# Performance work log

Measured on AMD Instinct MI355X. Metric: run time of the kernel, lower is better.

## Reference

```python
import jax, jax.numpy as jnp
import numpy as np
import math

L, B, T, D, H, F = 4, 4, 2048, 1024, 1024, 256
R_MIN, R_MAX = 0.9, 0.99
MAX_PHASE = math.pi / 50  # hardcoded in LRU.__init__


def setup_inputs() -> dict:
    key = jax.random.key(0)
    ks = iter(jax.random.split(key, 32))
    inputs = jax.random.normal(next(ks), (B, T, F), dtype=jnp.float32)
    # input projection (torch Linear layout: W [out,in])
    lim = 1.0 / math.sqrt(F)
    W_in = jax.random.uniform(next(ks), (D, F), minval=-lim, maxval=lim, dtype=jnp.float32)
    b_in = jax.random.uniform(next(ks), (D,), minval=-lim, maxval=lim, dtype=jnp.float32)
    # per-layer LRU params (stacked over layer dim)
    u1 = jax.random.uniform(next(ks), (L, H), dtype=jnp.float32) * (1 - 1e-5) + 1e-5
    mag_sq = u1 * (R_MAX ** 2 - R_MIN ** 2) + R_MIN ** 2
    nu_log = jnp.log(-0.5 * jnp.log(mag_sq + 1e-5))
    u2 = jax.random.uniform(next(ks), (L, H), dtype=jnp.float32) * (1 - 1e-5) + 1e-5
    theta_log = jnp.log(MAX_PHASE * u2)
    B_re = jax.random.normal(next(ks), (L, H, D), dtype=jnp.float32) / math.sqrt(2 * D)
    B_im = jax.random.normal(next(ks), (L, H, D), dtype=jnp.float32) / math.sqrt(2 * D)
    C_re = jax.random.normal(next(ks), (L, D, H), dtype=jnp.float32) / math.sqrt(H)
    C_im = jax.random.normal(next(ks), (L, D, H), dtype=jnp.float32) / math.sqrt(H)
    D_diag = jax.random.normal(next(ks), (L, D), dtype=jnp.float32)
    # LayerNorm affine
    ln_scale = jnp.ones((L, D), dtype=jnp.float32)
    ln_bias = jnp.zeros((L, D), dtype=jnp.float32)
    # GLU output linears (torch layout [out,in])
    limd = 1.0 / math.sqrt(D)
    w1 = jax.random.uniform(next(ks), (L, D, D), minval=-limd, maxval=limd, dtype=jnp.float32)
    b1 = jax.random.uniform(next(ks), (L, D), minval=-limd, maxval=limd, dtype=jnp.float32)
    w2 = jax.random.uniform(next(ks), (L, D, D), minval=-limd, maxval=limd, dtype=jnp.float32)
    b2 = jax.random.uniform(next(ks), (L, D), minval=-limd, maxval=limd, dtype=jnp.float32)
    return {"inputs": inputs, "W_in": W_in, "b_in": b_in, "nu_log": nu_log,
            "theta_log": theta_log, "B_re": B_re, "B_im": B_im, "C_re": C_re,
            "C_im": C_im, "D_diag": D_diag, "ln_scale": ln_scale, "ln_bias": ln_bias,
            "w1": w1, "b1": b1, "w2": w2, "b2": b2}


def _layernorm(x, scale, bias, eps=1e-5):
    mu = jnp.mean(x, axis=-1, keepdims=True)
    var = jnp.mean((x - mu) ** 2, axis=-1, keepdims=True)
    return (x - mu) * jax.lax.rsqrt(var + eps) * scale + bias


def _lru(x, nu_log, theta_log, B_re, B_im, C_re, C_im, D_diag):
    # x: [B,T,D] real -> [B,T,D] real
    nu = jnp.exp(nu_log)
    theta = jnp.exp(theta_log)
    lam = jnp.exp(-nu + 1j * theta)                        # [H] complex
    # gamma recomputed from nu_log each forward (matches torch code)
    gamma = jnp.exp(0.5 * jnp.log(1 - jnp.exp(-2 * nu) + 1e-5))
    B_norm = (B_re + 1j * B_im) * gamma[:, None]           # [H,D]
    Bu = jnp.einsum('hd,btd->bth', B_norm, x.astype(jnp.complex64))  # [B,T,H]

    def step(h, bu):
        h = lam * h + bu
        return h, h

    h0 = jnp.zeros((x.shape[0], lam.shape[0]), dtype=jnp.complex64)
    _, hs = jax.lax.scan(step, h0, jnp.swapaxes(Bu, 0, 1))  # [T,B,H]
    hs = jnp.swapaxes(hs, 0, 1)                             # [B,T,H]
    C = C_re + 1j * C_im                                    # [D,H]
    y = jnp.einsum('bth,dh->btd', hs, C).real + x * D_diag
    return y.astype(jnp.float32)


def reference(inputs, W_in, b_in, nu_log, theta_log, B_re, B_im, C_re, C_im,
              D_diag, ln_scale, ln_bias, w1, b1, w2, b2):
    x = inputs @ W_in.T + b_in                              # [B,T,D]
    n_layers = nu_log.shape[0]
    for l in range(n_layers):
        xn = _layernorm(x, ln_scale[l], ln_bias[l])
        y = _lru(xn, nu_log[l], theta_log[l], B_re[l], B_im[l],
                 C_re[l], C_im[l], D_diag[l])
        y = jax.nn.gelu(y, approximate=False)
        y = (y @ w1[l].T + b1[l]) * jax.nn.sigmoid(y @ w2[l].T + b2[l])
        x = x + y
    return x
```

## Files before the change

### kernel.cpp

```cpp
#include <hip/hip_runtime.h>
#include <hip/hip_bf16.h>
#include <math.h>

typedef unsigned short u16;
typedef short s16x8 __attribute__((ext_vector_type(8)));
typedef float f32x4 __attribute__((ext_vector_type(4)));
typedef unsigned short u16x4 __attribute__((ext_vector_type(4)));

#define NLAYER 4
#define BB 4
#define TT 2048
#define DD 1024
#define HH 1024
#define FF 256
#define MM 8192
#define CL 64
#define NC 32
#define PLANE 4096
#define STPLANE 131072

__device__ __forceinline__ u16 f2bf(float f) {
  __hip_bfloat16 h = __float2bfloat16(f);
  return __builtin_bit_cast(u16, h);
}
__device__ __forceinline__ float bf2f(u16 u) {
  __hip_bfloat16 h = __builtin_bit_cast(__hip_bfloat16, u);
  return __bfloat162float(h);
}

__global__ __launch_bounds__(256) void params_kernel(
    const float* __restrict__ nu_log, const float* __restrict__ theta_log,
    float* __restrict__ P) {
  int i = blockIdx.x * 256 + threadIdx.x;
  if (i >= PLANE) return;
  float nu = expf(nu_log[i]);
  float th = expf(theta_log[i]);
  float r = expf(-nu);
  P[i]           = r * cosf(th);
  P[PLANE + i]   = r * sinf(th);
  P[2*PLANE + i] = sqrtf(1.f - expf(-2.f * nu) + 1e-5f);
  float rC = expf(-(float)CL * nu);
  float thC = (float)CL * th;
  P[3*PLANE + i] = rC * cosf(thC);
  P[4*PLANE + i] = rC * sinf(thC);
}

__global__ __launch_bounds__(256) void f2bf_kernel(
    const float* __restrict__ src, u16* __restrict__ dst, int n) {
  int i = blockIdx.x * 256 + threadIdx.x;
  if (i < n) dst[i] = f2bf(src[i]);
}

__global__ __launch_bounds__(256) void conv_layer_kernel(
    const float* __restrict__ Bre, const float* __restrict__ Bim,
    const float* __restrict__ Cre, const float* __restrict__ Cim,
    const float* __restrict__ w1, const float* __restrict__ w2,
    const float* __restrict__ gamma,
    u16* __restrict__ wBn, u16* __restrict__ wC,
    u16* __restrict__ w1b, u16* __restrict__ w2b) {
  int idx = blockIdx.x * 256 + threadIdx.x;
  if (idx < 2097152) {
    int n = idx >> 10, d = idx & 1023;
    float v = (n < 1024) ? Bre[n * 1024 + d] * gamma[n]
                         : Bim[(n - 1024) * 1024 + d] * gamma[n - 1024];
    wBn[idx] = f2bf(v);
  } else if (idx < 4194304) {
    int i = idx - 2097152;
    int d = i >> 11, k = i & 2047;
    float v = (k < 1024) ? Cre[d * 1024 + k] : -Cim[d * 1024 + (k - 1024)];
    wC[i] = f2bf(v);
  } else if (idx < 5242880) {
    int i = idx - 4194304;
    w1b[i] = f2bf(w1[i]);
  } else if (idx < 6291456) {
    int i = idx - 5242880;
    w2b[i] = f2bf(w2[i]);
  }
}

__global__ __launch_bounds__(256) void ln_kernel(
    const float* __restrict__ x, const float* __restrict__ sc,
    const float* __restrict__ bi, u16* __restrict__ xn) {
  const int row = blockIdx.x;
  const int tid = threadIdx.x;
  const float4 v = ((const float4*)(x + (size_t)row * 1024))[tid];
  float s = v.x + v.y + v.z + v.w;
  float ss = v.x * v.x + v.y * v.y + v.z * v.z + v.w * v.w;
  __shared__ float r1[256], r2[256];
  r1[tid] = s; r2[tid] = ss;
  __syncthreads();
  for (int stp = 128; stp > 0; stp >>= 1) {
    if (tid < stp) { r1[tid] += r1[tid + stp]; r2[tid] += r2[tid + stp]; }
    __syncthreads();
  }
  const float mu = r1[0] * 0.0009765625f;
  const float var = r2[0] * 0.0009765625f - mu * mu;
  const float inv = rsqrtf(var + 1e-5f);
  const int c = tid * 4;
  u16x4 o;
  o.x = f2bf((v.x - mu) * inv * sc[c]     + bi[c]);
  o.y = f2bf((v.y - mu) * inv * sc[c + 1] + bi[c + 1]);
  o.z = f2bf((v.z - mu) * inv * sc[c + 2] + bi[c + 2]);
  o.w = f2bf((v.w - mu) * inv * sc[c + 3] + bi[c + 3]);
  *(u16x4*)&xn[(size_t)row * 1024 + c] = o;
}

__global__ __launch_bounds__(256) void scanA_kernel(
    u16* __restrict__ Bu, const float* __restrict__ P, float* __restrict__ st,
    int l) {
  const int tid = blockIdx.x * 256 + threadIdx.x;
  const int h2 = tid & 511;
  const int c = (tid >> 9) & 31;
  const int b = tid >> 14;
  const int h = h2 * 2;
  const float lr0 = P[l * 1024 + h],     li0 = P[PLANE + l * 1024 + h];
  const float lr1 = P[l * 1024 + h + 1], li1 = P[PLANE + l * 1024 + h + 1];
  const size_t base = ((size_t)(b * TT + c * CL)) * 2048 + h;
  float h0r = 0.f, h0i = 0.f, h1r = 0.f, h1i = 0.f;
  for (int j = 0; j < CL; j++) {
    size_t o = base + (size_t)j * 2048;
    uint re2 = *(const uint*)(Bu + o);
    uint im2 = *(const uint*)(Bu + o + 1024);
    float b0r = bf2f((u16)(re2 & 0xffffu)), b1r = bf2f((u16)(re2 >> 16));
    float b0i = bf2f((u16)(im2 & 0xffffu)), b1i = bf2f((u16)(im2 >> 16));
    float t0r = lr0 * h0r - li0 * h0i + b0r;
    float t0i = lr0 * h0i + li0 * h0r + b0i;
    float t1r = lr1 * h1r - li1 * h1i + b1r;
    float t1i = lr1 * h1i + li1 * h1r + b1i;
    h0r = t0r; h0i = t0i; h1r = t1r; h1i = t1i;
    *(uint*)(Bu + o)        = (uint)f2bf(h0r) | ((uint)f2bf(h1r) << 16);
    *(uint*)(Bu + o + 1024) = (uint)f2bf(h0i) | ((uint)f2bf(h1i) << 16);
  }
  size_t si = ((size_t)(b * NC + c)) * 1024 + h;
  st[si] = h0r; st[si + 1] = h1r;
  st[STPLANE + si] = h0i; st[STPLANE + si + 1] = h1i;
}

__global__ __launch_bounds__(256) void scanB_kernel(
    float* __restrict__ st, const float* __restrict__ P, int l) {
  const int tid = blockIdx.x * 256 + threadIdx.x;
  const int h = tid & 1023;
  const int b = tid >> 10;
  const float cr = P[3*PLANE + l * 1024 + h], ci = P[4*PLANE + l * 1024 + h];
  float pr = 0.f, pi = 0.f;
  for (int c = 0; c < NC; c++) {
    size_t i = ((size_t)(b * NC + c)) * 1024 + h;
    float sr = st[i], sim = st[STPLANE + i];
    st[i] = pr; st[STPLANE + i] = pi;
    float nr = cr * pr - ci * pi + sr;
    float ni = cr * pi + ci * pr + sim;
    pr = nr; pi = ni;
  }
}

__global__ __launch_bounds__(256) void scanC_kernel(
    u16* __restrict__ Bu, const float* __restrict__ P,
    const float* __restrict__ st, int l) {
  const int tid = blockIdx.x * 256 + threadIdx.x;
  const int h2 = tid & 511;
  const int c = (tid >> 9) & 31;
  const int b = tid >> 14;
  if (c == 0) return;
  const int h = h2 * 2;
  const float lr0 = P[l * 1024 + h],     li0 = P[PLANE + l * 1024 + h];
  const float lr1 = P[l * 1024 + h + 1], li1 = P[PLANE + l * 1024 + h + 1];
  size_t si = ((size_t)(b * NC + c)) * 1024 + h;
  float q0r = st[si], q1r = st[si + 1];
  float q0i = st[STPLANE + si], q1i = st[STPLANE + si + 1];
  const size_t base = ((size_t)(b * TT + c * CL)) * 2048 + h;
  for (int j = 0; j < CL; j++) {
    float t0r = lr0 * q0r - li0 * q0i;
    float t0i = lr0 * q0i + li0 * q0r;
    float t1r = lr1 * q1r - li1 * q1i;
    float t1i = lr1 * q1i + li1 * q1r;
    q0r = t0r; q0i = t0i; q1r = t1r; q1i = t1i;
    size_t o = base + (size_t)j * 2048;
    uint re2 = *(const uint*)(Bu + o);
    uint im2 = *(const uint*)(Bu + o + 1024);
    float v0r = bf2f((u16)(re2 & 0xffffu)) + q0r;
    float v1r = bf2f((u16)(re2 >> 16))     + q1r;
    float v0i = bf2f((u16)(im2 & 0xffffu)) + q0i;
    float v1i = bf2f((u16)(im2 >> 16))     + q1i;
    *(uint*)(Bu + o)        = (uint)f2bf(v0r) | ((uint)f2bf(v1r) << 16);
    *(uint*)(Bu + o + 1024) = (uint)f2bf(v0i) | ((uint)f2bf(v1i) << 16);
  }
}

__device__ __forceinline__ void stage_rows(const u16* __restrict__ gbase,
                                           int row_stride, u16* lds_base,
                                           int rows_per_wave, int wave,
                                           int lane) {
  const int r8 = lane >> 3;
  const int slot = lane & 7;
  const int gc = (slot ^ r8) * 8;
  #pragma unroll
  for (int i = 0; i < rows_per_wave / 8; i++) {
    const int rbase = wave * rows_per_wave + i * 8;
    const u16* g = gbase + (size_t)(rbase + r8) * row_stride + gc;
    u16* l = lds_base + rbase * 64;
    __builtin_amdgcn_global_load_lds(
        (const __attribute__((address_space(1))) void*)g,
        (__attribute__((address_space(3))) void*)l, 16, 0, 0);
  }
}

template <int MODE>
__global__ __launch_bounds__(256, 4) void gemm_kernel(
    const u16* __restrict__ A, const u16* __restrict__ W,
    const u16* __restrict__ W2, int K, int N, void* __restrict__ outp,
    const float* __restrict__ bias, const float* __restrict__ bias2,
    const float* __restrict__ ddiag, const u16* __restrict__ xnp) {
  __shared__ u16 As[128 * 64];
  __shared__ u16 Bs[64 * 64];
  __shared__ u16 Bs2[(MODE == 3) ? 64 * 64 : 64];

  const int tid = threadIdx.x;
  const int m0 = blockIdx.x * 128;
  const int n0 = blockIdx.y * 64;
  const int wave = tid >> 6;
  const int lane = tid & 63;
  const int wm = wave & 1;
  const int wn = wave >> 1;
  const int lr = lane & 15;
  const int quad = lane >> 4;
  const int sw = lr & 7;

  f32x4 acc[4][2];
  f32x4 acc2[4][2];
  #pragma unroll
  for (int i = 0; i < 4; i++)
    #pragma unroll
    for (int j = 0; j < 2; j++)
      #pragma unroll
      for (int r = 0; r < 4; r++) {
        acc[i][j][r] = 0.f;
        if constexpr (MODE == 3) acc2[i][j][r] = 0.f;
      }

  for (int kb = 0; kb < K; kb += 64) {
    stage_rows(A + (size_t)m0 * K + kb, K, As, 32, wave, lane);
    stage_rows(W + (size_t)n0 * K + kb, K, Bs, 16, wave, lane);
    if constexpr (MODE == 3)
      stage_rows(W2 + (size_t)n0 * K + kb, K, Bs2, 16, wave, lane);
    __syncthreads();
    #pragma unroll
    for (int ks = 0; ks < 2; ks++) {
      const int cslot = ((ks * 4 + quad) ^ sw) * 8;
      s16x8 af[4], bfr[2], bfr2[2];
      #pragma unroll
      for (int t = 0; t < 4; t++)
        af[t] = *(const s16x8*)&As[(wm * 64 + t * 16 + lr) * 64 + cslot];
      #pragma unroll
      for (int t = 0; t < 2; t++) {
        bfr[t] = *(const s16x8*)&Bs[(wn * 32 + t * 16 + lr) * 64 + cslot];
        if constexpr (MODE == 3)
          bfr2[t] = *(const s16x8*)&Bs2[(wn * 32 + t * 16 + lr) * 64 + cslot];
      }
      #pragma unroll
      for (int mt = 0; mt < 4; mt++)
        #pragma unroll
        for (int nt = 0; nt < 2; nt++) {
          acc[mt][nt] = __builtin_amdgcn_mfma_f32_16x16x32_bf16(
              af[mt], bfr[nt], acc[mt][nt], 0, 0, 0);
          if constexpr (MODE == 3)
            acc2[mt][nt] = __builtin_amdgcn_mfma_f32_16x16x32_bf16(
                af[mt], bfr2[nt], acc2[mt][nt], 0, 0, 0);
        }
    }
    __syncthreads();
  }

  const int mbase = m0 + wm * 64 + quad * 4;
  const int nbase = n0 + wn * 32 + lr;
  #pragma unroll
  for (int mt = 0; mt < 4; mt++)
    #pragma unroll
    for (int nt = 0; nt < 2; nt++) {
      const int n = nbase + nt * 16;
      #pragma unroll
      for (int r = 0; r < 4; r++) {
        const int m = mbase + mt * 16 + r;
        const float v = acc[mt][nt][r];
        if constexpr (MODE == 0) {
          ((u16*)outp)[(size_t)m * N + n] = f2bf(v);
        } else if constexpr (MODE == 1) {
          ((float*)outp)[(size_t)m * N + n] = v + bias[n];
        } else if constexpr (MODE == 2) {
          float t = v + bf2f(xnp[(size_t)m * 1024 + n]) * ddiag[n];
          float g = t * 0.5f * (1.f + erff(t * 0.70710678118f));
          ((u16*)outp)[(size_t)m * N + n] = f2bf(g);
        } else {
          float a = v + bias[n];
          float g2 = acc2[mt][nt][r] + bias2[n];
          float sig = 1.f / (1.f + expf(-g2));
          float* xp = (float*)outp;
          xp[(size_t)m * N + n] += a * sig;
        }
      }
    }
}

extern "C" void kernel_launch(void* const* d_in, const int* in_sizes, int n_in,
                              void* d_out, int out_size, void* d_ws,
                              size_t ws_size, hipStream_t stream) {
  const float* inputs    = (const float*)d_in[0];
  const float* W_in      = (const float*)d_in[1];
  const float* b_in      = (const float*)d_in[2];
  const float* nu_log    = (const float*)d_in[3];
  const float* theta_log = (const float*)d_in[4];
  const float* B_re      = (const float*)d_in[5];
  const float* B_im      = (const float*)d_in[6];
  const float* C_re      = (const float*)d_in[7];
  const float* C_im      = (const float*)d_in[8];
  const float* D_diag    = (const float*)d_in[9];
  const float* ln_s      = (const float*)d_in[10];
  const float* ln_b      = (const float*)d_in[11];
  const float* w1        = (const float*)d_in[12];
  const float* b1        = (const float*)d_in[13];
  const float* w2        = (const float*)d_in[14];
  const float* b2        = (const float*)d_in[15];
  float* x = (float*)d_out;

  char* p = (char*)d_ws;
  auto alloc = [&](size_t bytes) -> char* {
    char* r = p;
    p += (bytes + 255) & ~(size_t)255;
    return r;
  };
  float* P       = (float*)alloc(5 * PLANE * 4);
  u16* inputs_bf = (u16*)alloc((size_t)MM * FF * 2);
  u16* Win_bf    = (u16*)alloc((size_t)DD * FF * 2);
  u16* xn        = (u16*)alloc((size_t)MM * DD * 2);
  u16* Bu        = (u16*)alloc((size_t)MM * 2048 * 2);
  u16* yg        = (u16*)alloc((size_t)MM * DD * 2);
  float* st      = (float*)alloc(2 * (size_t)STPLANE * 4);
  u16* wBn       = (u16*)alloc((size_t)2048 * 1024 * 2);
  u16* wC        = (u16*)alloc((size_t)1024 * 2048 * 2);
  u16* w1b       = (u16*)alloc((size_t)1024 * 1024 * 2);
  u16* w2b       = (u16*)alloc((size_t)1024 * 1024 * 2);

  params_kernel<<<16, 256, 0, stream>>>(nu_log, theta_log, P);
  f2bf_kernel<<<(MM * FF + 255) / 256, 256, 0, stream>>>(inputs, inputs_bf, MM * FF);
  f2bf_kernel<<<(DD * FF + 255) / 256, 256, 0, stream>>>(W_in, Win_bf, DD * FF);

  gemm_kernel<1><<<dim3(64, 16), 256, 0, stream>>>(
      inputs_bf, Win_bf, nullptr, FF, DD, x, b_in, nullptr, nullptr, nullptr);

  for (int l = 0; l < NLAYER; l++) {
    ln_kernel<<<MM, 256, 0, stream>>>(x, ln_s + l * 1024, ln_b + l * 1024, xn);
    conv_layer_kernel<<<24576, 256, 0, stream>>>(
        B_re + (size_t)l * 1048576, B_im + (size_t)l * 1048576,
        C_re + (size_t)l * 1048576, C_im + (size_t)l * 1048576,
        w1 + (size_t)l * 1048576, w2 + (size_t)l * 1048576,
        P + 2 * PLANE + l * 1024, wBn, wC, w1b, w2b);
    gemm_kernel<0><<<dim3(64, 32), 256, 0, stream>>>(
        xn, wBn, nullptr, DD, 2048, Bu, nullptr, nullptr, nullptr, nullptr);
    scanA_kernel<<<256, 256, 0, stream>>>(Bu, P, st, l);
    scanB_kernel<<<16, 256, 0, stream>>>(st, P, l);
    scanC_kernel<<<256, 256, 0, stream>>>(Bu, P, st, l);
    gemm_kernel<2><<<dim3(64, 16), 256, 0, stream>>>(
        Bu, wC, nullptr, 2048, DD, yg, nullptr, nullptr, D_diag + l * 1024, xn);
    gemm_kernel<3><<<dim3(64, 16), 256, 0, stream>>>(
        yg, w1b, w2b, DD, DD, x, b1 + l * 1024, b2 + l * 1024, nullptr, nullptr);
  }
}
```

Before: 954.5 us.

## Double-buffer GEMM LDS tiles, remap blocks to 1D grid, split GLU GEMM

The GEMM kernel now keeps two LDS buffers per operand and prefetches the next K tile while computing the current one, which drops one barrier per iteration. Blocks are launched on a flat 1D grid and remapped so that consecutive groups of blocks fall on different XCD-strided tile ranges, aiming at better L2 locality. The fused dual-weight GLU GEMM is split into two passes: a sigmoid-gate GEMM that writes bf16 into the Bu buffer, then a value GEMM that multiplies by the stored gate and accumulates into x. The split lowers register pressure but adds an extra activation round-trip, and launch bounds drop to 3 blocks per SM to fit the doubled LDS.

```diff
diff --git a/kernel.cpp b/kernel.cpp
--- a/kernel.cpp
+++ b/kernel.cpp
@@ -205,18 +205,23 @@
 }
 
 template <int MODE>
-__global__ __launch_bounds__(256, 4) void gemm_kernel(
+__global__ __launch_bounds__(256, 3) void gemm_kernel(
     const u16* __restrict__ A, const u16* __restrict__ W,
-    const u16* __restrict__ W2, int K, int N, void* __restrict__ outp,
-    const float* __restrict__ bias, const float* __restrict__ bias2,
+    int K, int N, void* __restrict__ outp,
+    const float* __restrict__ bias,
     const float* __restrict__ ddiag, const u16* __restrict__ xnp) {
-  __shared__ u16 As[128 * 64];
-  __shared__ u16 Bs[64 * 64];
-  __shared__ u16 Bs2[(MODE == 3) ? 64 * 64 : 64];
+  __shared__ u16 As[2][128 * 64];
+  __shared__ u16 Bs[2][64 * 64];
 
   const int tid = threadIdx.x;
-  const int m0 = blockIdx.x * 128;
-  const int n0 = blockIdx.y * 64;
+  const int total = gridDim.x;
+  const int per = total >> 3;
+  const int flat = blockIdx.x;
+  const int g2 = (flat & 7) * per + (flat >> 3);
+  const int NT = N >> 6;
+  const int m0 = (g2 / NT) * 128;
+  const int n0 = (g2 % NT) * 64;
+
   const int wave = tid >> 6;
   const int lane = tid & 63;
   const int wm = wave & 1;
@@ -226,48 +231,44 @@
   const int sw = lr & 7;
 
   f32x4 acc[4][2];
-  f32x4 acc2[4][2];
   #pragma unroll
   for (int i = 0; i < 4; i++)
     #pragma unroll
     for (int j = 0; j < 2; j++)
       #pragma unroll
-      for (int r = 0; r < 4; r++) {
-        acc[i][j][r] = 0.f;
-        if constexpr (MODE == 3) acc2[i][j][r] = 0.f;
-      }
-
-  for (int kb = 0; kb < K; kb += 64) {
-    stage_rows(A + (size_t)m0 * K + kb, K, As, 32, wave, lane);
-    stage_rows(W + (size_t)n0 * K + kb, K, Bs, 16, wave, lane);
-    if constexpr (MODE == 3)
-      stage_rows(W2 + (size_t)n0 * K + kb, K, Bs2, 16, wave, lane);
+      for (int r = 0; r < 4; r++) acc[i][j][r] = 0.f;
+
+  const u16* Abase = A + (size_t)m0 * K;
+  const u16* Wbase = W + (size_t)n0 * K;
+  const int KI = K >> 6;
+
+  stage_rows(Abase, K, As[0], 32, wave, lane);
+  stage_rows(Wbase, K, Bs[0], 16, wave, lane);
+
+  for (int ki = 0; ki < KI; ki++) {
+    const int cur = ki & 1;
     __syncthreads();
+    if (ki + 1 < KI) {
+      stage_rows(Abase + ((ki + 1) << 6), K, As[cur ^ 1], 32, wave, lane);
+      stage_rows(Wbase + ((ki + 1) << 6), K, Bs[cur ^ 1], 16, wave, lane);
+    }
     #pragma unroll
     for (int ks = 0; ks < 2; ks++) {
       const int cslot = ((ks * 4 + quad) ^ sw) * 8;
-      s16x8 af[4], bfr[2], bfr2[2];
+      s16x8 af[4], bfr[2];
       #pragma unroll
       for (int t = 0; t < 4; t++)
-        af[t] = *(const s16x8*)&As[(wm * 64 + t * 16 + lr) * 64 + cslot];
-      #pragma unroll
-      for (int t = 0; t < 2; t++) {
-        bfr[t] = *(const s16x8*)&Bs[(wn * 32 + t * 16 + lr) * 64 + cslot];
-        if constexpr (MODE == 3)
-          bfr2[t] = *(const s16x8*)&Bs2[(wn * 32 + t * 16 + lr) * 64 + cslot];
-      }
+        af[t] = *(const s16x8*)&As[cur][(wm * 64 + t * 16 + lr) * 64 + cslot];
+      #pragma unroll
+      for (int t = 0; t < 2; t++)
+        bfr[t] = *(const s16x8*)&Bs[cur][(wn * 32 + t * 16 + lr) * 64 + cslot];
       #pragma unroll
       for (int mt = 0; mt < 4; mt++)
         #pragma unroll
-        for (int nt = 0; nt < 2; nt++) {
+        for (int nt = 0; nt < 2; nt++)
           acc[mt][nt] = __builtin_amdgcn_mfma_f32_16x16x32_bf16(
               af[mt], bfr[nt], acc[mt][nt], 0, 0, 0);
-          if constexpr (MODE == 3)
-            acc2[mt][nt] = __builtin_amdgcn_mfma_f32_16x16x32_bf16(
-                af[mt], bfr2[nt], acc2[mt][nt], 0, 0, 0);
-        }
     }
-    __syncthreads();
   }
 
   const int mbase = m0 + wm * 64 + quad * 4;
@@ -289,12 +290,12 @@
           float t = v + bf2f(xnp[(size_t)m * 1024 + n]) * ddiag[n];
           float g = t * 0.5f * (1.f + erff(t * 0.70710678118f));
           ((u16*)outp)[(size_t)m * N + n] = f2bf(g);
+        } else if constexpr (MODE == 4) {
+          float sig = 1.f / (1.f + expf(-(v + bias[n])));
+          ((u16*)outp)[(size_t)m * N + n] = f2bf(sig);
         } else {
           float a = v + bias[n];
-          float g2 = acc2[mt][nt][r] + bias2[n];
-          float sig = 1.f / (1.f + expf(-g2));
-          float* xp = (float*)outp;
-          xp[(size_t)m * N + n] += a * sig;
+          ((float*)outp)[(size_t)m * N + n] += a * bf2f(xnp[(size_t)m * N + n]);
         }
       }
     }
@@ -338,13 +339,14 @@
   u16* wC        = (u16*)alloc((size_t)1024 * 2048 * 2);
   u16* w1b       = (u16*)alloc((size_t)1024 * 1024 * 2);
   u16* w2b       = (u16*)alloc((size_t)1024 * 1024 * 2);
+  u16* sg        = Bu;
 
   params_kernel<<<16, 256, 0, stream>>>(nu_log, theta_log, P);
   f2bf_kernel<<<(MM * FF + 255) / 256, 256, 0, stream>>>(inputs, inputs_bf, MM * FF);
   f2bf_kernel<<<(DD * FF + 255) / 256, 256, 0, stream>>>(W_in, Win_bf, DD * FF);
 
-  gemm_kernel<1><<<dim3(64, 16), 256, 0, stream>>>(
-      inputs_bf, Win_bf, nullptr, FF, DD, x, b_in, nullptr, nullptr, nullptr);
+  gemm_kernel<1><<<1024, 256, 0, stream>>>(
+      inputs_bf, Win_bf, FF, DD, x, b_in, nullptr, nullptr);
 
   for (int l = 0; l < NLAYER; l++) {
     ln_kernel<<<MM, 256, 0, stream>>>(x, ln_s + l * 1024, ln_b + l * 1024, xn);
@@ -353,14 +355,16 @@
         C_re + (size_t)l * 1048576, C_im + (size_t)l * 1048576,
         w1 + (size_t)l * 1048576, w2 + (size_t)l * 1048576,
         P + 2 * PLANE + l * 1024, wBn, wC, w1b, w2b);
-    gemm_kernel<0><<<dim3(64, 32), 256, 0, stream>>>(
-        xn, wBn, nullptr, DD, 2048, Bu, nullptr, nullptr, nullptr, nullptr);
+    gemm_kernel<0><<<2048, 256, 0, stream>>>(
+        xn, wBn, DD, 2048, Bu, nullptr, nullptr, nullptr);
     scanA_kernel<<<256, 256, 0, stream>>>(Bu, P, st, l);
     scanB_kernel<<<16, 256, 0, stream>>>(st, P, l);
     scanC_kernel<<<256, 256, 0, stream>>>(Bu, P, st, l);
-    gemm_kernel<2><<<dim3(64, 16), 256, 0, stream>>>(
-        Bu, wC, nullptr, 2048, DD, yg, nullptr, nullptr, D_diag + l * 1024, xn);
-    gemm_kernel<3><<<dim3(64, 16), 256, 0, stream>>>(
-        yg, w1b, w2b, DD, DD, x, b1 + l * 1024, b2 + l * 1024, nullptr, nullptr);
-  }
-}
+    gemm_kernel<2><<<1024, 256, 0, stream>>>(
+        Bu, wC, 2048, DD, yg, nullptr, D_diag + l * 1024, xn);
+    gemm_kernel<4><<<1024, 256, 0, stream>>>(
+        yg, w2b, DD, DD, sg, b2 + l * 1024, nullptr, nullptr);
+    gemm_kernel<5><<<1024, 256, 0, stream>>>(
+        yg, w1b, DD, DD, x, b1 + l * 1024, nullptr, sg);
+  }
+}
```

Measured after the change: 1.231 ms. +28.9%, slower.

## Use 2-wave GEMM blocks with 64x64 per-wave tiles and XCD-aware block remap

Applied to the files above, without the earlier changes.

Each GEMM block now runs 2 waves instead of 4, and each wave computes a 64x64 tile (4x4 MFMA subtiles) rather than 64x32, which raises the MFMA work per LDS fragment load. The 2D grid is flattened and remapped so that consecutive block groups land on the same XCD (flat&7 stride), improving L2 locality across the 8 chiplets. The larger per-wave tile raises register pressure, especially in MODE 3 where both acc arrays double. Halving the threads per block also doubles the staging work each thread does.

```diff
diff --git a/kernel.cpp b/kernel.cpp
--- a/kernel.cpp
+++ b/kernel.cpp
@@ -205,7 +205,7 @@
 }
 
 template <int MODE>
-__global__ __launch_bounds__(256, 4) void gemm_kernel(
+__global__ __launch_bounds__(128, (MODE == 3) ? 2 : 3) void gemm_kernel(
     const u16* __restrict__ A, const u16* __restrict__ W,
     const u16* __restrict__ W2, int K, int N, void* __restrict__ outp,
     const float* __restrict__ bias, const float* __restrict__ bias2,
@@ -215,51 +215,55 @@
   __shared__ u16 Bs2[(MODE == 3) ? 64 * 64 : 64];
 
   const int tid = threadIdx.x;
-  const int m0 = blockIdx.x * 128;
-  const int n0 = blockIdx.y * 64;
+  const int per = gridDim.x >> 3;
+  const int flat = blockIdx.x;
+  const int g2 = (flat & 7) * per + (flat >> 3);
+  const int NT = N >> 6;
+  const int m0 = (g2 / NT) * 128;
+  const int n0 = (g2 % NT) * 64;
+
   const int wave = tid >> 6;
   const int lane = tid & 63;
-  const int wm = wave & 1;
-  const int wn = wave >> 1;
   const int lr = lane & 15;
   const int quad = lane >> 4;
   const int sw = lr & 7;
 
-  f32x4 acc[4][2];
-  f32x4 acc2[4][2];
+  f32x4 acc[4][4];
+  f32x4 acc2[4][4];
   #pragma unroll
   for (int i = 0; i < 4; i++)
     #pragma unroll
-    for (int j = 0; j < 2; j++)
+    for (int j = 0; j < 4; j++)
       #pragma unroll
       for (int r = 0; r < 4; r++) {
         acc[i][j][r] = 0.f;
         if constexpr (MODE == 3) acc2[i][j][r] = 0.f;
       }
 
+  const u16* Abase = A + (size_t)m0 * K;
+  const u16* Wbase = W + (size_t)n0 * K;
+
   for (int kb = 0; kb < K; kb += 64) {
-    stage_rows(A + (size_t)m0 * K + kb, K, As, 32, wave, lane);
-    stage_rows(W + (size_t)n0 * K + kb, K, Bs, 16, wave, lane);
+    stage_rows(Abase + kb, K, As, 64, wave, lane);
+    stage_rows(Wbase + kb, K, Bs, 32, wave, lane);
     if constexpr (MODE == 3)
-      stage_rows(W2 + (size_t)n0 * K + kb, K, Bs2, 16, wave, lane);
+      stage_rows(W2 + (size_t)n0 * K + kb, K, Bs2, 32, wave, lane);
     __syncthreads();
     #pragma unroll
     for (int ks = 0; ks < 2; ks++) {
       const int cslot = ((ks * 4 + quad) ^ sw) * 8;
-      s16x8 af[4], bfr[2], bfr2[2];
+      s16x8 af[4], bfr[4], bfr2[4];
       #pragma unroll
-      for (int t = 0; t < 4; t++)
-        af[t] = *(const s16x8*)&As[(wm * 64 + t * 16 + lr) * 64 + cslot];
-      #pragma unroll
-      for (int t = 0; t < 2; t++) {
-        bfr[t] = *(const s16x8*)&Bs[(wn * 32 + t * 16 + lr) * 64 + cslot];
+      for (int t = 0; t < 4; t++) {
+        af[t]  = *(const s16x8*)&As[(wave * 64 + t * 16 + lr) * 64 + cslot];
+        bfr[t] = *(const s16x8*)&Bs[(t * 16 + lr) * 64 + cslot];
         if constexpr (MODE == 3)
-          bfr2[t] = *(const s16x8*)&Bs2[(wn * 32 + t * 16 + lr) * 64 + cslot];
+          bfr2[t] = *(const s16x8*)&Bs2[(t * 16 + lr) * 64 + cslot];
       }
       #pragma unroll
       for (int mt = 0; mt < 4; mt++)
         #pragma unroll
-        for (int nt = 0; nt < 2; nt++) {
+        for (int nt = 0; nt < 4; nt++) {
           acc[mt][nt] = __builtin_amdgcn_mfma_f32_16x16x32_bf16(
               af[mt], bfr[nt], acc[mt][nt], 0, 0, 0);
           if constexpr (MODE == 3)
@@ -270,12 +274,12 @@
     __syncthreads();
   }
 
-  const int mbase = m0 + wm * 64 + quad * 4;
-  const int nbase = n0 + wn * 32 + lr;
+  const int mbase = m0 + wave * 64 + quad * 4;
+  const int nbase = n0 + lr;
   #pragma unroll
   for (int mt = 0; mt < 4; mt++)
     #pragma unroll
-    for (int nt = 0; nt < 2; nt++) {
+    for (int nt = 0; nt < 4; nt++) {
       const int n = nbase + nt * 16;
       #pragma unroll
       for (int r = 0; r < 4; r++) {
@@ -293,8 +297,7 @@
           float a = v + bias[n];
           float g2 = acc2[mt][nt][r] + bias2[n];
           float sig = 1.f / (1.f + expf(-g2));
-          float* xp = (float*)outp;
-          xp[(size_t)m * N + n] += a * sig;
+          ((float*)outp)[(size_t)m * N + n] += a * sig;
         }
       }
     }
@@ -343,7 +346,7 @@
   f2bf_kernel<<<(MM * FF + 255) / 256, 256, 0, stream>>>(inputs, inputs_bf, MM * FF);
   f2bf_kernel<<<(DD * FF + 255) / 256, 256, 0, stream>>>(W_in, Win_bf, DD * FF);
 
-  gemm_kernel<1><<<dim3(64, 16), 256, 0, stream>>>(
+  gemm_kernel<1><<<1024, 128, 0, stream>>>(
       inputs_bf, Win_bf, nullptr, FF, DD, x, b_in, nullptr, nullptr, nullptr);
 
   for (int l = 0; l < NLAYER; l++) {
@@ -353,14 +356,14 @@
         C_re + (size_t)l * 1048576, C_im + (size_t)l * 1048576,
         w1 + (size_t)l * 1048576, w2 + (size_t)l * 1048576,
         P + 2 * PLANE + l * 1024, wBn, wC, w1b, w2b);
-    gemm_kernel<0><<<dim3(64, 32), 256, 0, stream>>>(
+    gemm_kernel<0><<<2048, 128, 0, stream>>>(
         xn, wBn, nullptr, DD, 2048, Bu, nullptr, nullptr, nullptr, nullptr);
     scanA_kernel<<<256, 256, 0, stream>>>(Bu, P, st, l);
     scanB_kernel<<<16, 256, 0, stream>>>(st, P, l);
     scanC_kernel<<<256, 256, 0, stream>>>(Bu, P, st, l);
-    gemm_kernel<2><<<dim3(64, 16), 256, 0, stream>>>(
+    gemm_kernel<2><<<1024, 128, 0, stream>>>(
         Bu, wC, nullptr, 2048, DD, yg, nullptr, nullptr, D_diag + l * 1024, xn);
-    gemm_kernel<3><<<dim3(64, 16), 256, 0, stream>>>(
+    gemm_kernel<3><<<1024, 128, 0, stream>>>(
         yg, w1b, w2b, DD, DD, x, b1 + l * 1024, b2 + l * 1024, nullptr, nullptr);
   }
 }
```

Result: slower. 1.050 ms (+10.0%).
